# Optimization experiments

Hardware: AMD Instinct MI355X
Metric: run time of the kernel (lower is better)

## Reference

```python
import jax, jax.numpy as jnp
import numpy as np


def setup_inputs() -> dict:
    key = jax.random.key(0)
    k1, k2 = jax.random.split(key)
    H, W, C = 1024, 2048, 32
    img = jax.random.normal(k1, (1, C, H, W), dtype=jnp.float32)
    flow = jax.random.normal(k2, (1, 2, H, W), dtype=jnp.float32)
    return {"img": img, "flow": flow, "H": H, "W": W}


def reference(img, flow, H, W):
    # img: [1, C, H, W], flow: [1, 2, H, W]
    C = img.shape[1]
    u = flow[:, 0, :, :]  # [1, H, W]
    v = flow[:, 1, :, :]
    grid_x = jnp.arange(W, dtype=jnp.float32)[None, None, :]  # [1,1,W]
    grid_y = jnp.arange(H, dtype=jnp.float32)[None, :, None]  # [1,H,1]
    x = grid_x + u  # [1, H, W]
    y = grid_y + v
    # normalize to [-1, 1] then back (faithful to original two-step mapping)
    x = 2.0 * (x / (W - 1) - 0.5)
    y = 2.0 * (y / (H - 1) - 0.5)
    x = (x + 1.0) * 0.5 * (W - 1)
    y = (y + 1.0) * 0.5 * (H - 1)

    x0 = jnp.floor(x)
    x1 = x0 + 1.0
    y0 = jnp.floor(y)
    y1 = y0 + 1.0
    x0c = jnp.clip(x0, 0, W - 1).astype(jnp.int32)
    x1c = jnp.clip(x1, 0, W - 1).astype(jnp.int32)
    y0c = jnp.clip(y0, 0, H - 1).astype(jnp.int32)
    y1c = jnp.clip(y1, 0, H - 1).astype(jnp.int32)

    # bilinear weights from UNCLAMPED coords (as in the original)
    wa = (x1 - x) * (y1 - y)
    wb = (x1 - x) * (y - y0)
    wc = (x - x0) * (y1 - y)
    wd = (x - x0) * (y - y0)

    img_flat = jnp.transpose(img[0], (1, 2, 0)).reshape(H * W, C)  # [H*W, C]

    def gather_pixel(ix, iy):
        idx = (iy * W + ix).reshape(-1)  # [H*W]
        return jnp.take(img_flat, idx, axis=0)  # [H*W, C]

    Ia = gather_pixel(x0c, y0c)
    Ib = gather_pixel(x0c, y1c)
    Ic = gather_pixel(x1c, y0c)
    Id = gather_pixel(x1c, y1c)

    out = (Ia * wa.reshape(-1, 1) + Ib * wb.reshape(-1, 1)
           + Ic * wc.reshape(-1, 1) + Id * wd.reshape(-1, 1))  # [H*W, C]
    out = out.reshape(1, H, W, C)
    return jnp.transpose(out, (0, 3, 1, 2))  # [1, C, H, W]
```

## Files before the change

### kernel.cpp

```cpp
#include <hip/hip_runtime.h>


#define TSX 64
#define TSY 32
#define RAD 8
#define LW  80
#define LH  48
#define PLANE (LW*LH)
#define CGB 2
#define NV (LH*(LW/4))
#define NTHREADS 1024

#define GLOAD_LDS16(g, l)                                                  \
    __builtin_amdgcn_global_load_lds(                                      \
        (const __attribute__((address_space(1))) void*)(g),                \
        (__attribute__((address_space(3))) void*)(l), 16, 0, 0)

__global__ __launch_bounds__(NTHREADS, 8) void warp_pipe(
    const float* __restrict__ img,
    const float* __restrict__ flow,
    const int* __restrict__ Hp,
    const int* __restrict__ Wp,
    float* __restrict__ out,
    int HW, int C)
{
    __shared__ __align__(16) float lds[2][CGB * PLANE];

    const int W = *Wp;
    const int H = *Hp;
    const int tilesX = (W + TSX - 1) / TSX;
    const int tilesY = (H + TSY - 1) / TSY;
    const int ntiles = tilesX * tilesY;
    const int bid = blockIdx.x;
    if (bid >= ntiles) return;

    const int q = ntiles >> 3, r = ntiles & 7;
    const int xcd = bid & 7, sub = bid >> 3;
    const int t = (xcd < r ? xcd * (q + 1) : r * (q + 1) + (xcd - r) * q) + sub;

    const int tileY = t / tilesX;
    const int tileX = t - tileY * tilesX;
    const int gx0 = tileX * TSX - RAD;
    const int gy0 = tileY * TSY - RAD;

    const int tid = threadIdx.x;
    const int lx  = tid & 63;
    const int rw  = (tid >> 6) * 2;
    const int gx  = tileX * TSX + lx;

    const float Wm1 = (float)(W - 1);
    const float Hm1 = (float)(H - 1);

    float wtl[2], wth[2], wbl[2], wbh[2];
    int   enc[2], pixk[2];
    #pragma unroll
    for (int k = 0; k < 2; ++k) {
        const int gy = tileY * TSY + rw + k;
        enc[k] = -2;
        if (gx >= W || gy >= H) continue;
        const int pix = gy * W + gx;
        pixk[k] = pix;
        const float u = flow[pix];
        const float v = flow[HW + pix];

        const float x = (float)gx + u;
        const float y = (float)gy + v;
        const float x0 = floorf(x), x1 = x0 + 1.0f;
        const float y0 = floorf(y), y1 = y0 + 1.0f;

        const int x0c = (int)fminf(fmaxf(x0, 0.0f), Wm1);
        const int x1c = (int)fminf(fmaxf(x1, 0.0f), Wm1);
        const int y0c = (int)fminf(fmaxf(y0, 0.0f), Hm1);
        const int y1c = (int)fminf(fmaxf(y1, 0.0f), Hm1);

        const float wa = (x1 - x) * (y1 - y);
        const float wb = (x1 - x) * (y - y0);
        const float wc = (x - x0) * (y1 - y);
        const float wd = (x - x0) * (y - y0);

        const int pbx = min(x0c, W - 2);
        const int pby = min(y0c, H - 2);

        const float wlt = (x0c == pbx ? wa : 0.f) + (x1c == pbx ? wc : 0.f);
        const float wht = (x0c != pbx ? wa : 0.f) + (x1c != pbx ? wc : 0.f);
        const float wlb = (x0c == pbx ? wb : 0.f) + (x1c == pbx ? wd : 0.f);
        const float whb = (x0c != pbx ? wb : 0.f) + (x1c != pbx ? wd : 0.f);
        const bool t0 = (y0c == pby), t1 = (y1c == pby);
        wtl[k] = (t0 ? wlt : 0.f) + (t1 ? wlb : 0.f);
        wth[k] = (t0 ? wht : 0.f) + (t1 ? whb : 0.f);
        wbl[k] = (t0 ? 0.f : wlt) + (t1 ? 0.f : wlb);
        wbh[k] = (t0 ? 0.f : wht) + (t1 ? 0.f : whb);

        const int lxp = pbx - gx0;
        const int lyb = pby - gy0;
        enc[k] = (lxp >= 0 && lxp <= LW - 2 && lyb >= 0 && lyb <= LH - 2)
               ? (lyb * LW + lxp) : -1;
    }

    const int nph = (C + CGB - 1) / CGB;

    for (int i = tid; i < CGB * NV; i += NTHREADS) {
        const int ch  = i / NV;
        const int rem = i - ch * NV;
        const int rr  = rem / (LW / 4);
        const int g   = rem - rr * (LW / 4);
        const int yy  = min(max(gy0 + rr, 0), H - 1);
        const int xs  = min(max(gx0 + 4 * g, 0), W - 4);
        const int chc = min(ch, C - 1);
        GLOAD_LDS16(img + (size_t)chc * HW + (size_t)yy * W + xs,
                    &lds[0][i * 4]);
    }

    int buf = 0;
    for (int p = 0; p < nph; ++p) {
        __syncthreads();

        const int c0 = p * CGB;

        if (p + 1 < nph) {
            const int c0n = (p + 1) * CGB;
            float* dst = &lds[buf ^ 1][0];
            for (int i = tid; i < CGB * NV; i += NTHREADS) {
                const int ch  = i / NV;
                const int rem = i - ch * NV;
                const int rr  = rem / (LW / 4);
                const int g   = rem - rr * (LW / 4);
                const int yy  = min(max(gy0 + rr, 0), H - 1);
                const int xs  = min(max(gx0 + 4 * g, 0), W - 4);
                const int chc = min(c0n + ch, C - 1);
                GLOAD_LDS16(img + (size_t)chc * HW + (size_t)yy * W + xs,
                            dst + i * 4);
            }
        }

        const float* base = &lds[buf][0];
        #pragma unroll
        for (int k = 0; k < 2; ++k) {
            const int e = enc[k];
            if (e == -2) continue;

            if (__builtin_expect(e >= 0, 1)) {
                const float* b0 = base + e;
                #pragma unroll
                for (int c = 0; c < CGB; ++c) {
                    if (c0 + c >= C) break;
                    const float lt = b0[c * PLANE],      ht = b0[c * PLANE + 1];
                    const float lb = b0[c * PLANE + LW], hb = b0[c * PLANE + LW + 1];
                    out[(size_t)(c0 + c) * HW + pixk[k]] =
                        wtl[k] * lt + wth[k] * ht + wbl[k] * lb + wbh[k] * hb;
                }
            } else {
                const int pix = pixk[k];
                const int gy  = tileY * TSY + rw + k;
                const float u = flow[pix];
                const float v = flow[HW + pix];
                const float x = (float)gx + u;
                const float y = (float)gy + v;
                const float x0 = floorf(x), y0f = floorf(y);
                const int x0c = (int)fminf(fmaxf(x0, 0.0f), Wm1);
                const int x1c = (int)fminf(fmaxf(x0 + 1.0f, 0.0f), Wm1);
                const int y0c = (int)fminf(fmaxf(y0f, 0.0f), Hm1);
                const int y1c = (int)fminf(fmaxf(y0f + 1.0f, 0.0f), Hm1);
                const float wa = (x0 + 1.0f - x) * (y0f + 1.0f - y);
                const float wb = (x0 + 1.0f - x) * (y - y0f);
                const float wc = (x - x0) * (y0f + 1.0f - y);
                const float wd = (x - x0) * (y - y0f);
                for (int c = 0; c < CGB && c0 + c < C; ++c) {
                    const float* ic = img + (size_t)(c0 + c) * HW;
                    const float Ia = ic[(size_t)y0c * W + x0c];
                    const float Ib = ic[(size_t)y1c * W + x0c];
                    const float Ic = ic[(size_t)y0c * W + x1c];
                    const float Id = ic[(size_t)y1c * W + x1c];
                    out[(size_t)(c0 + c) * HW + pix] = wa*Ia + wb*Ib + wc*Ic + wd*Id;
                }
            }
        }
        buf ^= 1;
    }
}

extern "C" void kernel_launch(void* const* d_in, const int* in_sizes, int n_in,
                              void* d_out, int out_size, void* d_ws, size_t ws_size,
                              hipStream_t stream) {
    const float* img  = (const float*)d_in[0];
    const float* flow = (const float*)d_in[1];
    const int*   Hp   = (const int*)d_in[2];
    const int*   Wp   = (const int*)d_in[3];
    float* out = (float*)d_out;

    const int HW = in_sizes[1] / 2;
    const int C  = in_sizes[0] / HW;

    const int grid = (HW + TSX * TSY - 1) / (TSX * TSY) + 64;
    warp_pipe<<<grid, NTHREADS, 0, stream>>>(img, flow, Hp, Wp, out, HW, C);
}
```

Measured before the change: 132.3 us.

## Shrink halo, precompute staging addresses, and use partial vmcnt waits

Reduces the tile halo radius from 8 to 4, which cuts the LDS staging per channel pair and the redundant halo loads from global memory. Staging addresses are computed once per thread as two fixed slots instead of being recomputed with divisions in every phase. The full __syncthreads is replaced by an s_waitcnt vmcnt(4) plus a raw s_barrier so the prefetch of the next channel pair overlaps the gather. A scalar-load fallback handles edge tiles. The smaller halo sends more pixels to the slow global-gather path when the flow is large, and the hand-placed waitcnt relies on the exact count of outstanding loads.

After: 128.4 us (median of 3 runs). 3.0% less time.

```diff
diff --git a/kernel.cpp b/kernel.cpp
--- a/kernel.cpp
+++ b/kernel.cpp
@@ -3,20 +3,25 @@
 
 #define TSX 64
 #define TSY 32
-#define RAD 8
-#define LW  80
-#define LH  48
+#define RAD 4
+#define LW  (TSX + 2*RAD)
+#define LH  (TSY + 2*RAD)
+#define GPR (LW/4)
 #define PLANE (LW*LH)
+#define NV  (LH*GPR)
 #define CGB 2
-#define NV (LH*(LW/4))
+#define NSTG (CGB*NV)
 #define NTHREADS 1024
+#define SOFF (NSTG - NTHREADS)
+
+static_assert(NSTG >= NTHREADS && NSTG <= 2*NTHREADS, "2 slots per thread");
 
 #define GLOAD_LDS16(g, l)                                                  \
     __builtin_amdgcn_global_load_lds(                                      \
         (const __attribute__((address_space(1))) void*)(g),                \
         (__attribute__((address_space(3))) void*)(l), 16, 0, 0)
 
-__global__ __launch_bounds__(NTHREADS, 8) void warp_pipe(
+__global__ __launch_bounds__(NTHREADS, 8) void warp_pipe3(
     const float* __restrict__ img,
     const float* __restrict__ flow,
     const int* __restrict__ Hp,
@@ -24,7 +29,7 @@
     float* __restrict__ out,
     int HW, int C)
 {
-    __shared__ __align__(16) float lds[2][CGB * PLANE];
+    __shared__ __align__(16) float lds[2 * CGB * PLANE];
 
     const int W = *Wp;
     const int H = *Hp;
@@ -36,7 +41,7 @@
 
     const int q = ntiles >> 3, r = ntiles & 7;
     const int xcd = bid & 7, sub = bid >> 3;
-    const int t = (xcd < r ? xcd * (q + 1) : r * (q + 1) + (xcd - r) * q) + sub;
+    const int t = (xcd < r ? xcd*(q+1) : r*(q+1) + (xcd-r)*q) + sub;
 
     const int tileY = t / tilesX;
     const int tileX = t - tileY * tilesX;
@@ -52,7 +57,7 @@
     const float Hm1 = (float)(H - 1);
 
     float wtl[2], wth[2], wbl[2], wbh[2];
-    int   enc[2], pixk[2];
+    int enc[2], pixk[2] = {0, 0};
     #pragma unroll
     for (int k = 0; k < 2; ++k) {
         const int gy = tileY * TSY + rw + k;
@@ -93,62 +98,46 @@
 
         const int lxp = pbx - gx0;
         const int lyb = pby - gy0;
-        enc[k] = (lxp >= 0 && lxp <= LW - 2 && lyb >= 0 && lyb <= LH - 2)
+        enc[k] = (lxp >= 0 && lxp <= LW-2 && lyb >= 0 && lyb <= LH-2)
                ? (lyb * LW + lxp) : -1;
     }
 
+    float* optr0 = out + pixk[0];
+    float* optr1 = out + pixk[1];
+
+    int spix[2], chrel[2], dst4[2];
+    #pragma unroll
+    for (int s = 0; s < 2; ++s) {
+        const int idx = tid + s * SOFF;
+        const int ch  = idx / NV;
+        const int rem = idx - ch * NV;
+        const int rr  = rem / GPR;
+        const int g   = rem - rr * GPR;
+        const int yy  = min(max(gy0 + rr, 0), H - 1);
+        const int xs  = min(max(gx0 + 4*g, 0), W - 4);
+        chrel[s] = ch;
+        spix[s]  = yy * W + xs;
+        dst4[s]  = idx * 4;
+    }
+
     const int nph = (C + CGB - 1) / CGB;
-
-    for (int i = tid; i < CGB * NV; i += NTHREADS) {
-        const int ch  = i / NV;
-        const int rem = i - ch * NV;
-        const int rr  = rem / (LW / 4);
-        const int g   = rem - rr * (LW / 4);
-        const int yy  = min(max(gy0 + rr, 0), H - 1);
-        const int xs  = min(max(gx0 + 4 * g, 0), W - 4);
-        const int chc = min(ch, C - 1);
-        GLOAD_LDS16(img + (size_t)chc * HW + (size_t)yy * W + xs,
-                    &lds[0][i * 4]);
-    }
-
-    int buf = 0;
-    for (int p = 0; p < nph; ++p) {
-        __syncthreads();
-
-        const int c0 = p * CGB;
-
-        if (p + 1 < nph) {
-            const int c0n = (p + 1) * CGB;
-            float* dst = &lds[buf ^ 1][0];
-            for (int i = tid; i < CGB * NV; i += NTHREADS) {
-                const int ch  = i / NV;
-                const int rem = i - ch * NV;
-                const int rr  = rem / (LW / 4);
-                const int g   = rem - rr * (LW / 4);
-                const int yy  = min(max(gy0 + rr, 0), H - 1);
-                const int xs  = min(max(gx0 + 4 * g, 0), W - 4);
-                const int chc = min(c0n + ch, C - 1);
-                GLOAD_LDS16(img + (size_t)chc * HW + (size_t)yy * W + xs,
-                            dst + i * 4);
-            }
-        }
-
-        const float* base = &lds[buf][0];
+    const bool fast = ((W & 3) == 0) && ((tileX+1)*TSX <= W)
+                   && ((tileY+1)*TSY <= H);
+
+    auto gather2 = [&](const float* cur, int c0) {
         #pragma unroll
         for (int k = 0; k < 2; ++k) {
             const int e = enc[k];
             if (e == -2) continue;
-
+            float* o = (k == 0) ? optr0 : optr1;
             if (__builtin_expect(e >= 0, 1)) {
-                const float* b0 = base + e;
-                #pragma unroll
-                for (int c = 0; c < CGB; ++c) {
-                    if (c0 + c >= C) break;
-                    const float lt = b0[c * PLANE],      ht = b0[c * PLANE + 1];
-                    const float lb = b0[c * PLANE + LW], hb = b0[c * PLANE + LW + 1];
-                    out[(size_t)(c0 + c) * HW + pixk[k]] =
-                        wtl[k] * lt + wth[k] * ht + wbl[k] * lb + wbh[k] * hb;
-                }
+                const float* b0 = cur + e;
+                const float a0 = wtl[k], a1 = wth[k];
+                const float a2 = wbl[k], a3 = wbh[k];
+                o[0] = a0*b0[0] + a1*b0[1] + a2*b0[LW] + a3*b0[LW+1];
+                if (c0 + 1 < C)
+                    o[HW] = a0*b0[PLANE]   + a1*b0[PLANE+1]
+                          + a2*b0[PLANE+LW] + a3*b0[PLANE+LW+1];
             } else {
                 const int pix = pixk[k];
                 const int gy  = tileY * TSY + rw + k;
@@ -157,25 +146,83 @@
                 const float x = (float)gx + u;
                 const float y = (float)gy + v;
                 const float x0 = floorf(x), y0f = floorf(y);
-                const int x0c = (int)fminf(fmaxf(x0, 0.0f), Wm1);
-                const int x1c = (int)fminf(fmaxf(x0 + 1.0f, 0.0f), Wm1);
-                const int y0c = (int)fminf(fmaxf(y0f, 0.0f), Hm1);
-                const int y1c = (int)fminf(fmaxf(y0f + 1.0f, 0.0f), Hm1);
-                const float wa = (x0 + 1.0f - x) * (y0f + 1.0f - y);
-                const float wb = (x0 + 1.0f - x) * (y - y0f);
-                const float wc = (x - x0) * (y0f + 1.0f - y);
+                const int x0c = (int)fminf(fmaxf(x0, 0.f), Wm1);
+                const int x1c = (int)fminf(fmaxf(x0 + 1.f, 0.f), Wm1);
+                const int y0c = (int)fminf(fmaxf(y0f, 0.f), Hm1);
+                const int y1c = (int)fminf(fmaxf(y0f + 1.f, 0.f), Hm1);
+                const float wa = (x0 + 1.f - x) * (y0f + 1.f - y);
+                const float wb = (x0 + 1.f - x) * (y - y0f);
+                const float wc = (x - x0) * (y0f + 1.f - y);
                 const float wd = (x - x0) * (y - y0f);
                 for (int c = 0; c < CGB && c0 + c < C; ++c) {
                     const float* ic = img + (size_t)(c0 + c) * HW;
-                    const float Ia = ic[(size_t)y0c * W + x0c];
-                    const float Ib = ic[(size_t)y1c * W + x0c];
-                    const float Ic = ic[(size_t)y0c * W + x1c];
-                    const float Id = ic[(size_t)y1c * W + x1c];
-                    out[(size_t)(c0 + c) * HW + pix] = wa*Ia + wb*Ib + wc*Ic + wd*Id;
+                    o[(size_t)c * HW] =
+                          wa * ic[(size_t)y0c*W + x0c] + wb * ic[(size_t)y1c*W + x0c]
+                        + wc * ic[(size_t)y0c*W + x1c] + wd * ic[(size_t)y1c*W + x1c];
                 }
             }
         }
-        buf ^= 1;
+    };
+
+    if (fast) {
+        #pragma unroll
+        for (int s = 0; s < 2; ++s) {
+            const int chc = min(chrel[s], C - 1);
+            GLOAD_LDS16(img + (size_t)chc * HW + spix[s], &lds[dst4[s]]);
+        }
+        asm volatile("s_waitcnt vmcnt(0)" ::: "memory");
+        __builtin_amdgcn_s_barrier();
+        __builtin_amdgcn_sched_barrier(0);
+
+        float* cur = &lds[0];
+        float* nxt = &lds[CGB * PLANE];
+
+        for (int p = 0; p < nph; ++p) {
+            const int c0 = p * CGB;
+
+            if (p + 1 < nph) {
+                const int c0n = c0 + CGB;
+                #pragma unroll
+                for (int s = 0; s < 2; ++s) {
+                    const int chc = min(c0n + chrel[s], C - 1);
+                    GLOAD_LDS16(img + (size_t)chc * HW + spix[s], nxt + dst4[s]);
+                }
+            }
+            __builtin_amdgcn_sched_barrier(0);
+
+            gather2(cur, c0);
+
+            __builtin_amdgcn_sched_barrier(0);
+
+            if (p + 1 < nph) {
+                asm volatile("s_waitcnt vmcnt(4)" ::: "memory");
+                __builtin_amdgcn_sched_barrier(0);
+                __builtin_amdgcn_s_barrier();
+                __builtin_amdgcn_sched_barrier(0);
+            }
+            float* tmp = cur; cur = nxt; nxt = tmp;
+            optr0 += (size_t)CGB * HW;
+            optr1 += (size_t)CGB * HW;
+        }
+    } else {
+        for (int p = 0; p < nph; ++p) {
+            const int c0 = p * CGB;
+            __syncthreads();
+            for (int i = tid; i < CGB * PLANE; i += NTHREADS) {
+                const int ch  = i / PLANE;
+                const int rem = i - ch * PLANE;
+                const int rr  = rem / LW;
+                const int cc  = rem - rr * LW;
+                const int yy  = min(max(gy0 + rr, 0), H - 1);
+                const int xx  = min(max(gx0 + cc, 0), W - 1);
+                const int chc = min(c0 + ch, C - 1);
+                lds[i] = img[(size_t)chc * HW + (size_t)yy * W + xx];
+            }
+            __syncthreads();
+            gather2(&lds[0], c0);
+            optr0 += (size_t)CGB * HW;
+            optr1 += (size_t)CGB * HW;
+        }
     }
 }
 
@@ -192,5 +239,5 @@
     const int C  = in_sizes[0] / HW;
 
     const int grid = (HW + TSX * TSY - 1) / (TSX * TSY) + 64;
-    warp_pipe<<<grid, NTHREADS, 0, stream>>>(img, flow, Hp, Wp, out, HW, C);
+    warp_pipe3<<<grid, NTHREADS, 0, stream>>>(img, flow, Hp, Wp, out, HW, C);
 }
```
